# Kernel optimization log

Hardware: AMD Instinct MI355X
Metric: run time of the kernel (lower is better)

Reference implementation:

```python
import jax, jax.numpy as jnp
import numpy as np

EPS_LN = 1e-6
STAB = 1e-3  # FAVOR+ relu-kernel numerical stabilizer

def layer_norm(x, gamma, beta):
    mu = jnp.mean(x, axis=-1, keepdims=True)
    var = jnp.mean(jnp.square(x - mu), axis=-1, keepdims=True)
    return (x - mu) * jax.lax.rsqrt(var + EPS_LN) * gamma + beta

def setup_inputs() -> dict:
    key = jax.random.key(0)
    B, L, E, H, F = 8, 2048, 1024, 16, 4096
    dh = E // H
    ks = jax.random.split(key, 12)
    s_attn = 1.0 / np.sqrt(E)
    s_ffn1 = 1.0 / np.sqrt(E)
    s_ffn2 = 1.0 / np.sqrt(F)
    return {
        "x": jax.random.normal(ks[0], (B, L, E), jnp.float32),
        "gamma1": jnp.ones((E,), jnp.float32),
        "beta1": jnp.zeros((E,), jnp.float32),
        "wq": jax.random.normal(ks[1], (E, H, dh), jnp.float32) * s_attn,
        "wk": jax.random.normal(ks[2], (E, H, dh), jnp.float32) * s_attn,
        "wv": jax.random.normal(ks[3], (E, H, dh), jnp.float32) * s_attn,
        "wo": jax.random.normal(ks[4], (H, dh, E), jnp.float32) * s_attn,
        "w1": jax.random.normal(ks[5], (E, F), jnp.float32) * s_ffn1,
        "b1": jnp.zeros((F,), jnp.float32),
        "w2": jax.random.normal(ks[6], (F, E), jnp.float32) * s_ffn2,
        "b2": jnp.zeros((E,), jnp.float32),
    }

def reference(x, gamma1, beta1, wq, wk, wv, wo, w1, b1, w2, b2):
    # ln_1 (layernorm1)
    ln1 = layer_norm(x, gamma1, beta1)
    # q/k/v head projections (bias-free DenseEinsum)
    q = jnp.einsum('ble,ehd->blhd', ln1, wq)
    k = jnp.einsum('ble,ehd->blhd', ln1, wk)
    v = jnp.einsum('ble,ehd->blhd', ln1, wv)
    # FAVOR+ relu kernel transformation (default, no projection matrix)
    qp = jax.nn.relu(q) + STAB  # [B,L,H,M]
    kp = jax.nn.relu(k) + STAB
    # non-causal linear attention: numerator and denominator
    kvs = jnp.einsum('blhm,blhd->bhmd', kp, v)          # [B,H,M,Dh]
    num = jnp.einsum('blhm,bhmd->blhd', qp, kvs)        # [B,L,H,Dh]
    ksum = jnp.sum(kp, axis=1)                          # [B,H,M]
    den = jnp.einsum('blhm,bhm->blh', qp, ksum)         # [B,L,H]
    att = num / den[..., None]
    attn_out = jnp.einsum('blhd,hde->ble', att, wo)
    add1 = attn_out + x
    # original code reuses layernorm1 here (layernorm2 unused)
    ln2 = layer_norm(add1, gamma1, beta1)
    h = jax.nn.gelu(jnp.einsum('ble,ef->blf', ln2, w1) + b1, approximate=False)
    out2 = jax.nn.gelu(jnp.einsum('blf,fe->ble', h, w2) + b2, approximate=False)
    # dropout is identity at inference
    return out2 + add1
```

## Files before the change

### kernel.cpp

```cpp
#include <hip/hip_runtime.h>
#include <hip/hip_bf16.h>
#include <math.h>

typedef float f32x4 __attribute__((ext_vector_type(4)));
typedef __bf16 bf16x8 __attribute__((ext_vector_type(8)));
typedef unsigned short u16x8 __attribute__((ext_vector_type(8)));
typedef unsigned short u16x4 __attribute__((ext_vector_type(4)));

__device__ __forceinline__ float bf2f(unsigned short u) {
    unsigned int x = ((unsigned int)u) << 16;
    float f; __builtin_memcpy(&f, &x, 4); return f;
}
__device__ __forceinline__ unsigned short f2bf(float f) {
    unsigned int x; __builtin_memcpy(&x, &f, 4);
    unsigned int r = x + 0x7fffu + ((x >> 16) & 1u);
    return (unsigned short)(r >> 16);
}
__device__ __forceinline__ float gelu_fast(float v) {
    float z2 = v * (1.5957691216f + 0.0713548162f * v * v);
    float e  = __expf(z2);
    float t  = 1.0f - 2.0f * __builtin_amdgcn_rcpf(1.0f + e);
    return 0.5f * v * (1.0f + t);
}
__device__ __forceinline__ void gload_lds16(const unsigned short* g, unsigned short* l) {
    __builtin_amdgcn_global_load_lds(
        (const __attribute__((address_space(1))) unsigned int*)g,
        (__attribute__((address_space(3))) unsigned int*)l, 16, 0, 0);
}

__global__ __launch_bounds__(256) void transpose_w(
    const float* __restrict__ in, unsigned short* __restrict__ out, int K, int N)
{
    __shared__ unsigned short tile[64][72];
    int nbn = N >> 6;
    int tk = (blockIdx.x / nbn) << 6;
    int tn = (blockIdx.x % nbn) << 6;
    int t = threadIdx.x;
    int r = t >> 2, c0 = (t & 3) * 16;
    #pragma unroll
    for (int i = 0; i < 16; i += 4) {
        float4 f = *(const float4*)(in + (size_t)(tk + r) * N + tn + c0 + i);
        tile[r][c0 + i + 0] = f2bf(f.x);
        tile[r][c0 + i + 1] = f2bf(f.y);
        tile[r][c0 + i + 2] = f2bf(f.z);
        tile[r][c0 + i + 3] = f2bf(f.w);
    }
    __syncthreads();
    u16x8 o0, o1;
    #pragma unroll
    for (int i = 0; i < 8; i++) { o0[i] = tile[c0 + i][r]; o1[i] = tile[c0 + 8 + i][r]; }
    *(u16x8*)(out + (size_t)(tn + r) * K + tk + c0)     = o0;
    *(u16x8*)(out + (size_t)(tn + r) * K + tk + c0 + 8) = o1;
}

__global__ __launch_bounds__(256) void ksum_kernel(
    const unsigned short* __restrict__ kpT, float* __restrict__ ksum)
{
    int idx = blockIdx.x * 4 + (threadIdx.x >> 6);
    int lane = threadIdx.x & 63;
    int b = idx >> 10, hm = idx & 1023;
    const unsigned short* src = kpT + (size_t)hm * 16384 + b * 2048;
    float s = 0.f;
    #pragma unroll
    for (int g = 0; g < 4; g++) {
        u16x8 v = *(const u16x8*)(src + g * 512 + lane * 8);
        #pragma unroll
        for (int q = 0; q < 8; q++) s += bf2f(v[q]);
    }
    #pragma unroll
    for (int o = 32; o > 0; o >>= 1) s += __shfl_down(s, o);
    if (lane == 0) ksum[idx] = s;
}

__global__ __launch_bounds__(256) void kvs_mfma(
    const unsigned short* __restrict__ vT, const unsigned short* __restrict__ kpT,
    float* __restrict__ pbuf)
{
    int blk = blockIdx.x;
    int bh = blk >> 2, sp = blk & 3;
    int b = bh >> 4, h = bh & 15;
    const unsigned short* Abase = vT  + (size_t)(h * 64) * 16384 + b * 2048 + sp * 512;
    const unsigned short* Bbase = kpT + (size_t)(h * 64) * 16384 + b * 2048 + sp * 512;
    __shared__ unsigned short Al[64 * 64];
    __shared__ unsigned short Bl[64 * 64];
    int t = threadIdx.x;
    int lane = t & 63, wid = t >> 6;
    int l15 = lane & 15, l4 = lane >> 4;
    int wr = wid >> 1, wc = wid & 1;
    f32x4 acc[2][2] = {};
    for (int k0 = 0; k0 < 512; k0 += 64) {
        #pragma unroll
        for (int i = 0; i < 2; i++) {
            int chunk = i * 256 + t;
            int row = chunk >> 3, c = (chunk & 7) * 8;
            u16x8 av = *(const u16x8*)(Abase + (size_t)row * 16384 + k0 + c);
            u16x8 bv = *(const u16x8*)(Bbase + (size_t)row * 16384 + k0 + c);
            int off = (row * 128 + c * 2) ^ ((row & 7) << 4);
            *(u16x8*)((char*)Al + off) = av;
            *(u16x8*)((char*)Bl + off) = bv;
        }
        __syncthreads();
        #pragma unroll
        for (int kh = 0; kh < 2; kh++) {
            bf16x8 af[2], bf[2];
            #pragma unroll
            for (int mi = 0; mi < 2; mi++) {
                int row = wr * 32 + mi * 16 + l15;
                int off = (row * 128 + (kh * 32 + l4 * 8) * 2) ^ ((row & 7) << 4);
                af[mi] = *(const bf16x8*)((const char*)Al + off);
            }
            #pragma unroll
            for (int ni = 0; ni < 2; ni++) {
                int row = wc * 32 + ni * 16 + l15;
                int off = (row * 128 + (kh * 32 + l4 * 8) * 2) ^ ((row & 7) << 4);
                bf[ni] = *(const bf16x8*)((const char*)Bl + off);
            }
            #pragma unroll
            for (int mi = 0; mi < 2; mi++)
                #pragma unroll
                for (int ni = 0; ni < 2; ni++)
                    acc[mi][ni] = __builtin_amdgcn_mfma_f32_16x16x32_bf16(af[mi], bf[ni], acc[mi][ni], 0, 0, 0);
        }
        __syncthreads();
    }
    float* pb = pbuf + ((size_t)sp * 128 + bh) * 4096;
    #pragma unroll
    for (int mi = 0; mi < 2; mi++)
        #pragma unroll
        for (int ni = 0; ni < 2; ni++)
            #pragma unroll
            for (int j = 0; j < 4; j++) {
                int d = wr * 32 + mi * 16 + l4 * 4 + j;
                int m = wc * 32 + ni * 16 + l15;
                pb[d * 64 + m] = acc[mi][ni][j];
            }
}

__global__ __launch_bounds__(256) void reduce4(
    const float* __restrict__ pbuf, float* __restrict__ out)
{
    int i = blockIdx.x * 256 + threadIdx.x;
    float4 s = ((const float4*)pbuf)[i];
    #pragma unroll
    for (int sp = 1; sp < 4; sp++) {
        float4 p = ((const float4*)(pbuf + (size_t)sp * 524288))[i];
        s.x += p.x; s.y += p.y; s.z += p.z; s.w += p.w;
    }
    ((float4*)out)[i] = s;
}

__global__ __launch_bounds__(256) void ln_kernel(
    const float* __restrict__ x, const float* __restrict__ gamma,
    const float* __restrict__ beta, unsigned short* __restrict__ out)
{
    int row = blockIdx.x;
    int t = threadIdx.x;
    float4 v = ((const float4*)(x + (size_t)row * 1024))[t];
    float s  = v.x + v.y + v.z + v.w;
    float s2 = v.x * v.x + v.y * v.y + v.z * v.z + v.w * v.w;
    #pragma unroll
    for (int o = 32; o > 0; o >>= 1) { s += __shfl_down(s, o); s2 += __shfl_down(s2, o); }
    __shared__ float red[8];
    if ((t & 63) == 0) { red[t >> 6] = s; red[4 + (t >> 6)] = s2; }
    __syncthreads();
    s  = red[0] + red[1] + red[2] + red[3];
    s2 = red[4] + red[5] + red[6] + red[7];
    float mu  = s * (1.0f / 1024.0f);
    float var = s2 * (1.0f / 1024.0f) - mu * mu;
    float rs  = rsqrtf(var + 1e-6f);
    float4 g  = ((const float4*)gamma)[t];
    float4 be = ((const float4*)beta)[t];
    u16x4 o4;
    o4[0] = f2bf((v.x - mu) * rs * g.x + be.x);
    o4[1] = f2bf((v.y - mu) * rs * g.y + be.y);
    o4[2] = f2bf((v.z - mu) * rs * g.z + be.z);
    o4[3] = f2bf((v.w - mu) * rs * g.w + be.w);
    *(u16x4*)(out + (size_t)row * 1024 + t * 4) = o4;
}

template <int EP>
__global__ __launch_bounds__(512) void gemm256(
    const unsigned short* __restrict__ A, const unsigned short* __restrict__ Bt,
    void* __restrict__ C, const float* __restrict__ bias,
    const float* __restrict__ addv, int M, int N, int K)
{
    __shared__ unsigned short ldsbuf[69632];
    const int nbn = N >> 8;
    const int nwg = (M >> 8) * nbn;
    int bid = blockIdx.x;
    int wg = (bid & 7) * (nwg >> 3) + (bid >> 3);
    int tm = wg / nbn, tn = wg % nbn;
    const int tid = threadIdx.x;
    const int lane = tid & 63;
    const int l15 = lane & 15, l4 = lane >> 4;
    const int wid = tid >> 6;
    const int wr = wid >> 2, wc = wid & 3;

    const unsigned short* Ab = A + (size_t)(tm << 8) * K;
    const unsigned short* Bb = Bt + (size_t)(tn << 8) * K;

    const int swz   = (l15 & 7) << 4;
    const int koff0 = (l4 * 16) ^ swz;
    const int koff1 = (64 + l4 * 16) ^ swz;
    const int arow  = wr * 16384 + l15 * 128;
    const int brow  = wc * 8192  + l15 * 128;

    int goff[4];
    #pragma unroll
    for (int i = 0; i < 4; i++) {
        int cid = i * 512 + tid;
        int row = cid >> 3, c = cid & 7;
        goff[i] = row * K + ((c ^ (row & 7)) << 3);
    }
    const int ld0 = tid * 8;

    f32x4 acc[8][4] = {};
    const int NT = K >> 6;

#define STAGE_TILE(kt, slot)                                                   \
    {                                                                          \
        int k0_ = (kt) << 6;                                                   \
        _Pragma("unroll")                                                      \
        for (int i_ = 0; i_ < 4; i_++) {                                       \
            gload_lds16(Ab + (size_t)(goff[i_] + k0_), ldsbuf + (slot) * 32768 + ld0 + i_ * 4096); \
            gload_lds16(Bb + (size_t)(goff[i_] + k0_), ldsbuf + (slot) * 32768 + 16384 + ld0 + i_ * 4096); \
        }                                                                      \
    }

#define TILE_STEP(t_, s_)                                                      \
    {                                                                          \
        if ((t_) + 1 < NT) STAGE_TILE((t_) + 1, (s_) ^ 1);                     \
        const char* As_ = (const char*)(ldsbuf + (s_) * 32768);                \
        const char* Bs_ = (const char*)(ldsbuf + (s_) * 32768 + 16384);        \
        bf16x8 a_[8], b_[4];                                                   \
        _Pragma("unroll")                                                      \
        for (int m = 0; m < 8; m++) a_[m] = *(const bf16x8*)(As_ + arow + m * 2048 + koff0); \
        _Pragma("unroll")                                                      \
        for (int n = 0; n < 4; n++) b_[n] = *(const bf16x8*)(Bs_ + brow + n * 2048 + koff0); \
        __builtin_amdgcn_s_setprio(1);                                         \
        _Pragma("unroll")                                                      \
        for (int m = 0; m < 8; m++)                                            \
            _Pragma("unroll")                                                  \
            for (int n = 0; n < 4; n++)                                        \
                acc[m][n] = __builtin_amdgcn_mfma_f32_16x16x32_bf16(a_[m], b_[n], acc[m][n], 0, 0, 0); \
        __builtin_amdgcn_s_setprio(0);                                         \
        _Pragma("unroll")                                                      \
        for (int m = 0; m < 8; m++) a_[m] = *(const bf16x8*)(As_ + arow + m * 2048 + koff1); \
        _Pragma("unroll")                                                      \
        for (int n = 0; n < 4; n++) b_[n] = *(const bf16x8*)(Bs_ + brow + n * 2048 + koff1); \
        __builtin_amdgcn_s_setprio(1);                                         \
        _Pragma("unroll")                                                      \
        for (int m = 0; m < 8; m++)                                            \
            _Pragma("unroll")                                                  \
            for (int n = 0; n < 4; n++)                                        \
                acc[m][n] = __builtin_amdgcn_mfma_f32_16x16x32_bf16(a_[m], b_[n], acc[m][n], 0, 0, 0); \
        __builtin_amdgcn_s_setprio(0);                                         \
        asm volatile("s_waitcnt vmcnt(0)" ::: "memory");                       \
        __builtin_amdgcn_s_barrier();                                          \
    }

    STAGE_TILE(0, 0);
    asm volatile("s_waitcnt vmcnt(0)" ::: "memory");
    __builtin_amdgcn_s_barrier();

    for (int t = 0; t < NT; t += 2) {
        TILE_STEP(t, 0);
        TILE_STEP(t + 1, 1);
    }
#undef TILE_STEP
#undef STAGE_TILE

    int rbase = (tm << 8) + wr * 128;
    int cbase = (tn << 8) + wc * 64;
    if constexpr (EP == 2 || EP == 4) {
        #pragma unroll
        for (int n = 0; n < 4; n++) {
            int col = cbase + n * 16 + l15;
            float bval = 0.f;
            if constexpr (EP == 4) bval = bias[col];
            #pragma unroll
            for (int mf = 0; mf < 8; mf++) {
                #pragma unroll
                for (int j = 0; j < 4; j++) {
                    int row = rbase + mf * 16 + l4 * 4 + j;
                    float val = acc[mf][n][j];
                    if constexpr (EP == 4) val = gelu_fast(val + bval);
                    ((float*)C)[(size_t)row * N + col] = val + addv[(size_t)row * N + col];
                }
            }
        }
    } else {
        unsigned short* myl = ldsbuf + wid * 8704;
        #pragma unroll
        for (int n = 0; n < 4; n++) {
            int col = cbase + n * 16 + l15;
            float bval = 0.f;
            if constexpr (EP == 3) bval = bias[col];
            #pragma unroll
            for (int mf = 0; mf < 8; mf++) {
                #pragma unroll
                for (int j = 0; j < 4; j++) {
                    float val = acc[mf][n][j];
                    if constexpr (EP == 1) val = fmaxf(val, 0.f) + 1e-3f;
                    if constexpr (EP == 3) val = gelu_fast(val + bval);
                    myl[(mf * 16 + l4 * 4 + j) * 68 + n * 16 + l15] = f2bf(val);
                }
            }
        }
        #pragma unroll
        for (int c = 0; c < 16; c++) {
            int lrow = c * 8 + (lane >> 3);
            int cc = (lane & 7) * 8;
            u16x4 lo = *(const u16x4*)(myl + lrow * 68 + cc);
            u16x4 hi = *(const u16x4*)(myl + lrow * 68 + cc + 4);
            unsigned short* dst = (unsigned short*)C + (size_t)(rbase + lrow) * N + cbase + cc;
            *(u16x4*)dst = lo;
            *(u16x4*)(dst + 4) = hi;
        }
    }
}

__global__ __launch_bounds__(256) void att_num_kernel(
    const unsigned short* __restrict__ qp, const float* __restrict__ kvsT,
    const float* __restrict__ ksum, unsigned short* __restrict__ att)
{
    int blk = blockIdx.x;
    int t16 = blk & 15, h = (blk >> 4) & 15, b = blk >> 8;
    __shared__ unsigned short Al[128 * 64];
    __shared__ unsigned short Bl[64 * 64];
    __shared__ float kss[64];
    int tid = threadIdx.x;
    int lane = tid & 63, wid = tid >> 6;
    int l15 = lane & 15, l4 = lane >> 4;
    const unsigned short* Ab = qp + ((size_t)(b * 2048 + t16 * 128)) * 1024 + h * 64;
    const float* Bb  = kvsT + (size_t)(b * 16 + h) * 4096;
    const float* ksb = ksum + (b * 16 + h) * 64;
    #pragma unroll
    for (int i = 0; i < 4; i++) {
        int chunk = tid + i * 256;
        int row = chunk >> 3, c = (chunk & 7) * 8;
        u16x8 av = *(const u16x8*)(Ab + (size_t)row * 1024 + c);
        int off = (row * 128 + c * 2) ^ ((row & 7) << 4);
        *(u16x8*)((char*)Al + off) = av;
    }
    #pragma unroll
    for (int i = 0; i < 2; i++) {
        int chunk = tid + i * 256;
        int row = chunk >> 3, c = (chunk & 7) * 8;
        const float* src = Bb + (size_t)row * 64 + c;
        u16x8 bv;
        #pragma unroll
        for (int q = 0; q < 8; q++) bv[q] = f2bf(src[q]);
        int off = (row * 128 + c * 2) ^ ((row & 7) << 4);
        *(u16x8*)((char*)Bl + off) = bv;
    }
    if (tid < 64) kss[tid] = ksb[tid];
    __syncthreads();

    f32x4 acc[2][4] = {};
    #pragma unroll
    for (int kk = 0; kk < 64; kk += 32) {
        bf16x8 af[2], bfr[4];
        #pragma unroll
        for (int m = 0; m < 2; m++) {
            int row = wid * 32 + m * 16 + l15;
            int off = (row * 128 + (kk + l4 * 8) * 2) ^ ((row & 7) << 4);
            af[m] = *(const bf16x8*)((const char*)Al + off);
        }
        #pragma unroll
        for (int n = 0; n < 4; n++) {
            int row = n * 16 + l15;
            int off = (row * 128 + (kk + l4 * 8) * 2) ^ ((row & 7) << 4);
            bfr[n] = *(const bf16x8*)((const char*)Bl + off);
        }
        #pragma unroll
        for (int m = 0; m < 2; m++)
            #pragma unroll
            for (int n = 0; n < 4; n++)
                acc[m][n] = __builtin_amdgcn_mfma_f32_16x16x32_bf16(af[m], bfr[n], acc[m][n], 0, 0, 0);
    }
    __syncthreads();

    #pragma unroll
    for (int m = 0; m < 2; m++) {
        #pragma unroll
        for (int j = 0; j < 4; j++) {
            int lrow = wid * 32 + m * 16 + l4 * 4 + j;
            float den = 0.f;
            #pragma unroll
            for (int mm = 0; mm < 64; mm += 8) {
                int off = (lrow * 128 + mm * 2) ^ ((lrow & 7) << 4);
                u16x8 a8 = *(const u16x8*)((const char*)Al + off);
                #pragma unroll
                for (int q = 0; q < 8; q++) den += bf2f(a8[q]) * kss[mm + q];
            }
            float rden = 1.0f / den;
            size_t grow = (size_t)(b * 2048 + t16 * 128 + lrow);
            #pragma unroll
            for (int n = 0; n < 4; n++) {
                int col = h * 64 + n * 16 + l15;
                att[grow * 1024 + col] = f2bf(acc[m][n][j] * rden);
            }
        }
    }
}

extern "C" void kernel_launch(void* const* d_in, const int* in_sizes, int n_in,
                              void* d_out, int out_size, void* d_ws, size_t ws_size,
                              hipStream_t stream) {
    (void)in_sizes; (void)n_in; (void)out_size; (void)ws_size;
    const float* x      = (const float*)d_in[0];
    const float* gamma1 = (const float*)d_in[1];
    const float* beta1  = (const float*)d_in[2];
    const float* wq     = (const float*)d_in[3];
    const float* wk     = (const float*)d_in[4];
    const float* wv     = (const float*)d_in[5];
    const float* wo     = (const float*)d_in[6];
    const float* w1     = (const float*)d_in[7];
    const float* b1     = (const float*)d_in[8];
    const float* w2     = (const float*)d_in[9];
    const float* b2     = (const float*)d_in[10];
    float* out = (float*)d_out;

    const size_t MB = 1024 * 1024;
    char* ws = (char*)d_ws;
    unsigned short* wq_bt = (unsigned short*)(ws + 0 * MB);
    unsigned short* wk_bt = (unsigned short*)(ws + 2 * MB);
    unsigned short* wv_bt = (unsigned short*)(ws + 4 * MB);
    unsigned short* wo_bt = (unsigned short*)(ws + 6 * MB);
    unsigned short* w1_bt = (unsigned short*)(ws + 8 * MB);
    unsigned short* w2_bt = (unsigned short*)(ws + 16 * MB);
    unsigned short* lnbuf = (unsigned short*)(ws + 24 * MB);
    float*          add1  = (float*)(ws + 56 * MB);
    float*          pbuf  = (float*)(ws + 88 * MB);
    unsigned short* qp    = (unsigned short*)(ws + 120 * MB);
    unsigned short* kpT   = (unsigned short*)(ws + 152 * MB);
    unsigned short* vT    = (unsigned short*)(ws + 184 * MB);
    float*          kvsT  = (float*)(ws + 216 * MB);
    float*          ksum  = (float*)(ws + 218 * MB);
    unsigned short* hbuf  = (unsigned short*)(ws + 120 * MB);

    dim3 blk(256), blk512(512);
    transpose_w<<<dim3(256),  blk, 0, stream>>>(wq, wq_bt, 1024, 1024);
    transpose_w<<<dim3(256),  blk, 0, stream>>>(wk, wk_bt, 1024, 1024);
    transpose_w<<<dim3(256),  blk, 0, stream>>>(wv, wv_bt, 1024, 1024);
    transpose_w<<<dim3(256),  blk, 0, stream>>>(wo, wo_bt, 1024, 1024);
    transpose_w<<<dim3(1024), blk, 0, stream>>>(w1, w1_bt, 1024, 4096);
    transpose_w<<<dim3(1024), blk, 0, stream>>>(w2, w2_bt, 4096, 1024);
    ln_kernel<<<dim3(16384), blk, 0, stream>>>(x, gamma1, beta1, lnbuf);
    gemm256<1><<<dim3(256), blk512, 0, stream>>>(lnbuf, wq_bt, qp, nullptr, nullptr, 16384, 1024, 1024);
    gemm256<1><<<dim3(256), blk512, 0, stream>>>(wk_bt, lnbuf, kpT, nullptr, nullptr, 1024, 16384, 1024);
    gemm256<0><<<dim3(256), blk512, 0, stream>>>(wv_bt, lnbuf, vT, nullptr, nullptr, 1024, 16384, 1024);
    ksum_kernel<<<dim3(2048), blk, 0, stream>>>(kpT, ksum);
    kvs_mfma<<<dim3(512), blk, 0, stream>>>(vT, kpT, pbuf);
    reduce4<<<dim3(512), blk, 0, stream>>>(pbuf, kvsT);
    att_num_kernel<<<dim3(2048), blk, 0, stream>>>(qp, kvsT, ksum, qp);
    gemm256<2><<<dim3(256), blk512, 0, stream>>>(qp, wo_bt, add1, nullptr, x, 16384, 1024, 1024);
    ln_kernel<<<dim3(16384), blk, 0, stream>>>(add1, gamma1, beta1, lnbuf);
    gemm256<3><<<dim3(1024), blk512, 0, stream>>>(lnbuf, w1_bt, hbuf, b1, nullptr, 16384, 4096, 1024);
    gemm256<4><<<dim3(256),  blk512, 0, stream>>>(hbuf, w2_bt, out, b2, add1, 16384, 1024, 4096);
}
```

Baseline: 652.2 us.

## Fuse K/V projections, ksum and split-K reduce; store residual in bf16

The separate K and V projection GEMMs become one GEMM with M=2048, relying on wk_bt and wv_bt being adjacent in the workspace and kpT/vT being adjacent in the output; the relu epilogue is applied only to the first half (tm<4). The ksum kernel is removed: ksum is built inside kvs_mfma from the staged kp tiles using atomics, after a memset. The reduce4 kernel is removed and att_num sums the four split partials when loading. The residual add1 is stored as bf16, halving its traffic, with a bf16-input layernorm. This cuts launches and memory traffic at the cost of lower residual precision and atomic nondeterminism.

Measured after the change: 593.5 us (median of 2 runs). -9.0%, faster.

```diff
diff --git a/kernel.cpp b/kernel.cpp
--- a/kernel.cpp
+++ b/kernel.cpp
@@ -53,28 +53,9 @@
     *(u16x8*)(out + (size_t)(tn + r) * K + tk + c0 + 8) = o1;
 }
 
-__global__ __launch_bounds__(256) void ksum_kernel(
-    const unsigned short* __restrict__ kpT, float* __restrict__ ksum)
-{
-    int idx = blockIdx.x * 4 + (threadIdx.x >> 6);
-    int lane = threadIdx.x & 63;
-    int b = idx >> 10, hm = idx & 1023;
-    const unsigned short* src = kpT + (size_t)hm * 16384 + b * 2048;
-    float s = 0.f;
-    #pragma unroll
-    for (int g = 0; g < 4; g++) {
-        u16x8 v = *(const u16x8*)(src + g * 512 + lane * 8);
-        #pragma unroll
-        for (int q = 0; q < 8; q++) s += bf2f(v[q]);
-    }
-    #pragma unroll
-    for (int o = 32; o > 0; o >>= 1) s += __shfl_down(s, o);
-    if (lane == 0) ksum[idx] = s;
-}
-
 __global__ __launch_bounds__(256) void kvs_mfma(
     const unsigned short* __restrict__ vT, const unsigned short* __restrict__ kpT,
-    float* __restrict__ pbuf)
+    float* __restrict__ pbuf, float* __restrict__ ksum)
 {
     int blk = blockIdx.x;
     int bh = blk >> 2, sp = blk & 3;
@@ -88,6 +69,7 @@
     int l15 = lane & 15, l4 = lane >> 4;
     int wr = wid >> 1, wc = wid & 1;
     f32x4 acc[2][2] = {};
+    float ks0 = 0.f, ks1 = 0.f;
     for (int k0 = 0; k0 < 512; k0 += 64) {
         #pragma unroll
         for (int i = 0; i < 2; i++) {
@@ -95,6 +77,10 @@
             int row = chunk >> 3, c = (chunk & 7) * 8;
             u16x8 av = *(const u16x8*)(Abase + (size_t)row * 16384 + k0 + c);
             u16x8 bv = *(const u16x8*)(Bbase + (size_t)row * 16384 + k0 + c);
+            float s = 0.f;
+            #pragma unroll
+            for (int q = 0; q < 8; q++) s += bf2f(bv[q]);
+            if (i == 0) ks0 += s; else ks1 += s;
             int off = (row * 128 + c * 2) ^ ((row & 7) << 4);
             *(u16x8*)((char*)Al + off) = av;
             *(u16x8*)((char*)Bl + off) = bv;
@@ -123,6 +109,12 @@
         }
         __syncthreads();
     }
+    #pragma unroll
+    for (int o = 4; o > 0; o >>= 1) { ks0 += __shfl_down(ks0, o); ks1 += __shfl_down(ks1, o); }
+    if ((t & 7) == 0) {
+        atomicAdd(&ksum[bh * 64 + (t >> 3)], ks0);
+        atomicAdd(&ksum[bh * 64 + 32 + (t >> 3)], ks1);
+    }
     float* pb = pbuf + ((size_t)sp * 128 + bh) * 4096;
     #pragma unroll
     for (int mi = 0; mi < 2; mi++)
@@ -134,19 +126,6 @@
                 int m = wc * 32 + ni * 16 + l15;
                 pb[d * 64 + m] = acc[mi][ni][j];
             }
-}
-
-__global__ __launch_bounds__(256) void reduce4(
-    const float* __restrict__ pbuf, float* __restrict__ out)
-{
-    int i = blockIdx.x * 256 + threadIdx.x;
-    float4 s = ((const float4*)pbuf)[i];
-    #pragma unroll
-    for (int sp = 1; sp < 4; sp++) {
-        float4 p = ((const float4*)(pbuf + (size_t)sp * 524288))[i];
-        s.x += p.x; s.y += p.y; s.z += p.z; s.w += p.w;
-    }
-    ((float4*)out)[i] = s;
 }
 
 __global__ __launch_bounds__(256) void ln_kernel(
@@ -178,11 +157,41 @@
     *(u16x4*)(out + (size_t)row * 1024 + t * 4) = o4;
 }
 
+__global__ __launch_bounds__(256) void ln_bf16_kernel(
+    const unsigned short* __restrict__ x, const float* __restrict__ gamma,
+    const float* __restrict__ beta, unsigned short* __restrict__ out)
+{
+    int row = blockIdx.x;
+    int t = threadIdx.x;
+    u16x4 uv = ((const u16x4*)(x + (size_t)row * 1024))[t];
+    float v0 = bf2f(uv[0]), v1 = bf2f(uv[1]), v2 = bf2f(uv[2]), v3 = bf2f(uv[3]);
+    float s  = v0 + v1 + v2 + v3;
+    float s2 = v0 * v0 + v1 * v1 + v2 * v2 + v3 * v3;
+    #pragma unroll
+    for (int o = 32; o > 0; o >>= 1) { s += __shfl_down(s, o); s2 += __shfl_down(s2, o); }
+    __shared__ float red[8];
+    if ((t & 63) == 0) { red[t >> 6] = s; red[4 + (t >> 6)] = s2; }
+    __syncthreads();
+    s  = red[0] + red[1] + red[2] + red[3];
+    s2 = red[4] + red[5] + red[6] + red[7];
+    float mu  = s * (1.0f / 1024.0f);
+    float var = s2 * (1.0f / 1024.0f) - mu * mu;
+    float rs  = rsqrtf(var + 1e-6f);
+    float4 g  = ((const float4*)gamma)[t];
+    float4 be = ((const float4*)beta)[t];
+    u16x4 o4;
+    o4[0] = f2bf((v0 - mu) * rs * g.x + be.x);
+    o4[1] = f2bf((v1 - mu) * rs * g.y + be.y);
+    o4[2] = f2bf((v2 - mu) * rs * g.z + be.z);
+    o4[3] = f2bf((v3 - mu) * rs * g.w + be.w);
+    *(u16x4*)(out + (size_t)row * 1024 + t * 4) = o4;
+}
+
 template <int EP>
 __global__ __launch_bounds__(512) void gemm256(
     const unsigned short* __restrict__ A, const unsigned short* __restrict__ Bt,
     void* __restrict__ C, const float* __restrict__ bias,
-    const float* __restrict__ addv, int M, int N, int K)
+    const void* __restrict__ addv, int M, int N, int K)
 {
     __shared__ unsigned short ldsbuf[69632];
     const int nbn = N >> 8;
@@ -272,37 +281,40 @@
 
     int rbase = (tm << 8) + wr * 128;
     int cbase = (tn << 8) + wc * 64;
-    if constexpr (EP == 2 || EP == 4) {
+    if constexpr (EP == 4) {
+        const unsigned short* av16 = (const unsigned short*)addv;
+        #pragma unroll
+        for (int n = 0; n < 4; n++) {
+            int col = cbase + n * 16 + l15;
+            float bval = bias[col];
+            #pragma unroll
+            for (int mf = 0; mf < 8; mf++) {
+                #pragma unroll
+                for (int j = 0; j < 4; j++) {
+                    int row = rbase + mf * 16 + l4 * 4 + j;
+                    float val = gelu_fast(acc[mf][n][j] + bval);
+                    ((float*)C)[(size_t)row * N + col] = val + bf2f(av16[(size_t)row * N + col]);
+                }
+            }
+        }
+    } else {
+        const float* avf = (const float*)addv;
+        unsigned short* myl = ldsbuf + wid * 8704;
         #pragma unroll
         for (int n = 0; n < 4; n++) {
             int col = cbase + n * 16 + l15;
             float bval = 0.f;
-            if constexpr (EP == 4) bval = bias[col];
+            if constexpr (EP == 3) bval = bias[col];
             #pragma unroll
             for (int mf = 0; mf < 8; mf++) {
                 #pragma unroll
                 for (int j = 0; j < 4; j++) {
                     int row = rbase + mf * 16 + l4 * 4 + j;
                     float val = acc[mf][n][j];
-                    if constexpr (EP == 4) val = gelu_fast(val + bval);
-                    ((float*)C)[(size_t)row * N + col] = val + addv[(size_t)row * N + col];
-                }
-            }
-        }
-    } else {
-        unsigned short* myl = ldsbuf + wid * 8704;
-        #pragma unroll
-        for (int n = 0; n < 4; n++) {
-            int col = cbase + n * 16 + l15;
-            float bval = 0.f;
-            if constexpr (EP == 3) bval = bias[col];
-            #pragma unroll
-            for (int mf = 0; mf < 8; mf++) {
-                #pragma unroll
-                for (int j = 0; j < 4; j++) {
-                    float val = acc[mf][n][j];
                     if constexpr (EP == 1) val = fmaxf(val, 0.f) + 1e-3f;
+                    if constexpr (EP == 5) { if (tm < 4) val = fmaxf(val, 0.f) + 1e-3f; }
                     if constexpr (EP == 3) val = gelu_fast(val + bval);
+                    if constexpr (EP == 2) val += avf[(size_t)row * N + col];
                     myl[(mf * 16 + l4 * 4 + j) * 68 + n * 16 + l15] = f2bf(val);
                 }
             }
@@ -321,11 +333,12 @@
 }
 
 __global__ __launch_bounds__(256) void att_num_kernel(
-    const unsigned short* __restrict__ qp, const float* __restrict__ kvsT,
+    const unsigned short* __restrict__ qp, const float* __restrict__ pbuf,
     const float* __restrict__ ksum, unsigned short* __restrict__ att)
 {
     int blk = blockIdx.x;
     int t16 = blk & 15, h = (blk >> 4) & 15, b = blk >> 8;
+    int bh = b * 16 + h;
     __shared__ unsigned short Al[128 * 64];
     __shared__ unsigned short Bl[64 * 64];
     __shared__ float kss[64];
@@ -333,8 +346,8 @@
     int lane = tid & 63, wid = tid >> 6;
     int l15 = lane & 15, l4 = lane >> 4;
     const unsigned short* Ab = qp + ((size_t)(b * 2048 + t16 * 128)) * 1024 + h * 64;
-    const float* Bb  = kvsT + (size_t)(b * 16 + h) * 4096;
-    const float* ksb = ksum + (b * 16 + h) * 64;
+    const float* Bb  = pbuf + (size_t)bh * 4096;
+    const float* ksb = ksum + bh * 64;
     #pragma unroll
     for (int i = 0; i < 4; i++) {
         int chunk = tid + i * 256;
@@ -347,10 +360,16 @@
     for (int i = 0; i < 2; i++) {
         int chunk = tid + i * 256;
         int row = chunk >> 3, c = (chunk & 7) * 8;
-        const float* src = Bb + (size_t)row * 64 + c;
+        float sum8[8] = {};
+        #pragma unroll
+        for (int sp = 0; sp < 4; sp++) {
+            const float* src = Bb + (size_t)sp * 524288 + row * 64 + c;
+            #pragma unroll
+            for (int q = 0; q < 8; q++) sum8[q] += src[q];
+        }
         u16x8 bv;
         #pragma unroll
-        for (int q = 0; q < 8; q++) bv[q] = f2bf(src[q]);
+        for (int q = 0; q < 8; q++) bv[q] = f2bf(sum8[q]);
         int off = (row * 128 + c * 2) ^ ((row & 7) << 4);
         *(u16x8*)((char*)Bl + off) = bv;
     }
@@ -431,12 +450,11 @@
     unsigned short* w1_bt = (unsigned short*)(ws + 8 * MB);
     unsigned short* w2_bt = (unsigned short*)(ws + 16 * MB);
     unsigned short* lnbuf = (unsigned short*)(ws + 24 * MB);
-    float*          add1  = (float*)(ws + 56 * MB);
+    unsigned short* add1b = (unsigned short*)(ws + 56 * MB);
     float*          pbuf  = (float*)(ws + 88 * MB);
     unsigned short* qp    = (unsigned short*)(ws + 120 * MB);
     unsigned short* kpT   = (unsigned short*)(ws + 152 * MB);
     unsigned short* vT    = (unsigned short*)(ws + 184 * MB);
-    float*          kvsT  = (float*)(ws + 216 * MB);
     float*          ksum  = (float*)(ws + 218 * MB);
     unsigned short* hbuf  = (unsigned short*)(ws + 120 * MB);
 
@@ -449,14 +467,12 @@
     transpose_w<<<dim3(1024), blk, 0, stream>>>(w2, w2_bt, 4096, 1024);
     ln_kernel<<<dim3(16384), blk, 0, stream>>>(x, gamma1, beta1, lnbuf);
     gemm256<1><<<dim3(256), blk512, 0, stream>>>(lnbuf, wq_bt, qp, nullptr, nullptr, 16384, 1024, 1024);
-    gemm256<1><<<dim3(256), blk512, 0, stream>>>(wk_bt, lnbuf, kpT, nullptr, nullptr, 1024, 16384, 1024);
-    gemm256<0><<<dim3(256), blk512, 0, stream>>>(wv_bt, lnbuf, vT, nullptr, nullptr, 1024, 16384, 1024);
-    ksum_kernel<<<dim3(2048), blk, 0, stream>>>(kpT, ksum);
-    kvs_mfma<<<dim3(512), blk, 0, stream>>>(vT, kpT, pbuf);
-    reduce4<<<dim3(512), blk, 0, stream>>>(pbuf, kvsT);
-    att_num_kernel<<<dim3(2048), blk, 0, stream>>>(qp, kvsT, ksum, qp);
-    gemm256<2><<<dim3(256), blk512, 0, stream>>>(qp, wo_bt, add1, nullptr, x, 16384, 1024, 1024);
-    ln_kernel<<<dim3(16384), blk, 0, stream>>>(add1, gamma1, beta1, lnbuf);
+    gemm256<5><<<dim3(512), blk512, 0, stream>>>(wk_bt, lnbuf, kpT, nullptr, nullptr, 2048, 16384, 1024);
+    hipMemsetAsync(ksum, 0, 32 * 1024, stream);
+    kvs_mfma<<<dim3(512), blk, 0, stream>>>(vT, kpT, pbuf, ksum);
+    att_num_kernel<<<dim3(2048), blk, 0, stream>>>(qp, pbuf, ksum, qp);
+    gemm256<2><<<dim3(256), blk512, 0, stream>>>(qp, wo_bt, add1b, nullptr, x, 16384, 1024, 1024);
+    ln_bf16_kernel<<<dim3(16384), blk, 0, stream>>>(add1b, gamma1, beta1, lnbuf);
     gemm256<3><<<dim3(1024), blk512, 0, stream>>>(lnbuf, w1_bt, hbuf, b1, nullptr, 16384, 4096, 1024);
-    gemm256<4><<<dim3(256),  blk512, 0, stream>>>(hbuf, w2_bt, out, b2, add1, 16384, 1024, 4096);
-}
+    gemm256<4><<<dim3(256),  blk512, 0, stream>>>(hbuf, w2_bt, out, b2, add1b, 16384, 1024, 4096);
+}
```
